# Performance work log

Hardware: AMD Instinct MI355X
Metric: run time of the kernel (lower is better)

Reference implementation:

```python
import jax, jax.numpy as jnp
import numpy as np

B, L, HID = 4, 2048, 2048
H, D = 16, 128
BASE = 10000.0
NEG = -1e30


def _rope_tables(seq_len, dim, dtype):
    # inv_freq: (dim/2,), emb = concat(freqs, freqs): (L, dim)
    inv_freq = 1.0 / (BASE ** (jnp.arange(0, dim, 2, dtype=jnp.float32) / dim))
    t = jnp.arange(seq_len, dtype=jnp.float32)
    freqs = t[:, None] * inv_freq[None, :]          # (L, dim/2)
    emb = jnp.concatenate([freqs, freqs], axis=-1)  # (L, dim)
    return jnp.cos(emb).astype(dtype), jnp.sin(emb).astype(dtype)


def _rotate_half(x):
    x1, x2 = x[..., : x.shape[-1] // 2], x[..., x.shape[-1] // 2 :]
    return jnp.concatenate([-x2, x1], axis=-1)


def setup_inputs() -> dict:
    key = jax.random.key(0)
    k1, k2, k3 = jax.random.split(key, 3)
    x = jax.random.normal(k1, (B, L, HID), dtype=jnp.float32)
    # qkv init std = sqrt(2/(5*hidden)); fc xavier std ~ sqrt(2/(in+out))
    Wqkv = jax.random.normal(k2, (HID, 3 * H * D), dtype=jnp.float32) * np.sqrt(2.0 / (5.0 * HID))
    Wo = jax.random.normal(k3, (H * D, HID), dtype=jnp.float32) * np.sqrt(2.0 / (H * D + HID))
    return {"x": x, "Wqkv": Wqkv, "Wo": Wo}


def reference(x, Wqkv, Wo):
    b, l, _ = x.shape
    qkv = (x @ Wqkv).reshape(b, l, 3, H, D).transpose(2, 0, 3, 1, 4)  # (3,b,h,l,d)
    q, k, v = qkv[0], qkv[1], qkv[2]
    cos, sin = _rope_tables(l, D, x.dtype)  # (l, D) each, broadcasts over (b,h,l,d)
    q = q * cos + _rotate_half(q) * sin
    k = k * cos + _rotate_half(k) * sin
    scale = 1.0 / np.sqrt(D)
    scores = jnp.einsum("bhqd,bhkd->bhqk", q, k) * scale  # (b,h,l,l)
    causal = jnp.tril(jnp.ones((l, l), dtype=bool))
    scores = jnp.where(causal, scores, NEG)
    att = jax.nn.softmax(scores, axis=-1)
    out = jnp.einsum("bhqk,bhkd->bhqd", att, v)  # (b,h,l,d)
    out = out.transpose(0, 2, 1, 3).reshape(b, l, H * D)
    return out @ Wo
```

## Files before the change

kernel.cpp:

```cpp
#include <hip/hip_runtime.h>
#include <hip/hip_bf16.h>
#include <stdint.h>

typedef unsigned short ushort_t;
typedef __bf16 bf16x8 __attribute__((ext_vector_type(8)));
typedef float    f32x4 __attribute__((ext_vector_type(4)));
typedef float   f32x16 __attribute__((ext_vector_type(16)));
typedef unsigned short us4 __attribute__((ext_vector_type(4)));
typedef unsigned int ui4 __attribute__((ext_vector_type(4)));

#define QK_SCALE 0.12751744f
#define NEG_BIG  -1e30f

#define BARRIER() do { asm volatile("" ::: "memory"); __builtin_amdgcn_s_barrier(); asm volatile("" ::: "memory"); } while (0)
#define VMCNT(N)  asm volatile("s_waitcnt vmcnt(" #N ")" ::: "memory")
#define MFMA16(d, a, b) d = __builtin_amdgcn_mfma_f32_16x16x32_bf16(a, b, d, 0, 0, 0)

__device__ __forceinline__ unsigned short f2bf(float f) {
    union { float f; unsigned int u; } v; v.f = f;
    unsigned int u = v.u;
    return (unsigned short)((u + 0x7FFFu + ((u >> 16) & 1u)) >> 16);
}

__device__ __forceinline__ unsigned int pk2bf(float a, float b) {
    unsigned int r;
    asm("v_cvt_pk_bf16_f32 %0, %1, %2" : "=v"(r) : "v"(a), "v"(b));
    return r;
}

__device__ __forceinline__ void gload16(const void* g, void* l) {
    __builtin_amdgcn_global_load_lds(
        (__attribute__((address_space(1))) void*)(uintptr_t)g,
        (__attribute__((address_space(3))) void*)(uint32_t)(uintptr_t)l,
        16, 0, 0);
}


__global__ __launch_bounds__(256) void cvt_bf16_kernel(
    const float4* __restrict__ in, us4* __restrict__ out, int n4) {
    int i = blockIdx.x * 256 + threadIdx.x;
    if (i >= n4) return;
    float4 v = in[i];
    us4 o; o[0] = f2bf(v.x); o[1] = f2bf(v.y); o[2] = f2bf(v.z); o[3] = f2bf(v.w);
    out[i] = o;
}

__global__ __launch_bounds__(256) void transpose_bf16(
    const float* __restrict__ in, ushort_t* __restrict__ out, int R, int C) {
    __shared__ float t[64][65];
    int c0 = blockIdx.x * 64, r0 = blockIdx.y * 64;
    int cc = threadIdx.x & 63, rr = threadIdx.x >> 6;
#pragma unroll
    for (int i = 0; i < 16; ++i) {
        int r = i * 4 + rr;
        t[r][cc] = in[(size_t)(r0 + r) * C + c0 + cc];
    }
    __syncthreads();
#pragma unroll
    for (int i = 0; i < 16; ++i) {
        int r = i * 4 + rr;
        out[(size_t)(c0 + r) * R + r0 + cc] = f2bf(t[cc][r]);
    }
}

__global__ __launch_bounds__(256) void transpose_wqkv(
    const float* __restrict__ in , ushort_t* __restrict__ out ) {
    __shared__ float t[64][65];
    int c0 = blockIdx.x * 64, r0 = blockIdx.y * 64;
    int cc = threadIdx.x & 63, rr = threadIdx.x >> 6;
    int n = c0 + cc;
    int which = n >> 11;
    int src = n;
    if (which < 2) {
        int h = (n >> 7) & 15, p = n & 127;
        int po = (p & 15) | (((p >> 5) & 3) << 4) | (((p >> 4) & 1) << 6);
        src = (which << 11) + (h << 7) + po;
    }
#pragma unroll
    for (int i = 0; i < 16; ++i) {
        int r = i * 4 + rr;
        t[r][cc] = in[(size_t)(r0 + r) * 6144 + src];
    }
    __syncthreads();
#pragma unroll
    for (int i = 0; i < 16; ++i) {
        int r = i * 4 + rr;
        out[(size_t)(c0 + r) * 2048 + r0 + cc] = f2bf(t[cc][r]);
    }
}

__global__ __launch_bounds__(256) void rope_table_kernel(float2* __restrict__ rope) {
    int i = blockIdx.x * 256 + threadIdx.x;
    int l = i >> 6, j = i & 63;
    float inv = exp2f((float)j * -0.20762050593046f);
    float f = (float)l * inv;
    rope[i] = make_float2(cosf(f), sinf(f));
}


template <int EPI>
__global__ __launch_bounds__(512, 2)
void gemm256(const ushort_t* __restrict__ A, const ushort_t* __restrict__ Bt,
             int M, int N, int K,
             float* __restrict__ C,
             ushort_t* __restrict__ Qb, ushort_t* __restrict__ Kb,
             ushort_t* __restrict__ Vt, const float2* __restrict__ rope) {
    __shared__ __attribute__((aligned(16))) char lds[131072];

    const int tid  = threadIdx.x;
    const int lane = tid & 63, wid = tid >> 6;
    const int lr = lane & 15, lg = lane >> 4;
    const int wr = wid >> 2, wc = wid & 3;

    const int nbn = N >> 8;
    const int nwg = gridDim.x;
    const int bid = blockIdx.x;
    const int wg  = (bid & 7) * (nwg >> 3) + (bid >> 3);
    const int bm  = wg / nbn, bn = wg % nbn;

    const int srow = tid >> 3;
    const int scol = ((tid & 7) << 4) ^ ((srow & 7) << 4);
    const size_t rowK2 = (size_t)K * 2;
    const char* sA0 = (const char*)A + ((size_t)(bm * 256 + srow)) * rowK2 + scol;
    const char* sA1 = sA0 + 128 * rowK2;
    const char* sB0 = (const char*)Bt + ((size_t)(bn * 256 + srow)) * rowK2 + scol;
    const char* sB1 = sB0 + 128 * rowK2;

    auto stg = [&](const char* s, int ch, int kt, int dst) {
        gload16(s + (size_t)(ch * 64) * rowK2 + (size_t)kt * 128, lds + dst + wid * 1024);
    };

    const int xk0 = (lg * 16) ^ ((lr & 7) << 4);
    const int xk1 = (64 + lg * 16) ^ ((lr & 7) << 4);
    const int rowA = wr * 16384 + lr * 128;
    const int rowB = 32768 + (wc >> 1) * 16384 + ((wc & 1) * 64 + lr) * 128;

    auto rdA = [&](int bu, int mi, int kk) -> bf16x8 {
        return *(const bf16x8*)(lds + bu * 65536 + rowA + mi * 2048 + (kk ? xk1 : xk0));
    };
    auto rdB = [&](int bu, int ni, int kk) -> bf16x8 {
        return *(const bf16x8*)(lds + bu * 65536 + rowB + ni * 2048 + (kk ? xk1 : xk0));
    };

    f32x4 acc[8][4];
#pragma unroll
    for (int m = 0; m < 8; ++m)
#pragma unroll
        for (int n = 0; n < 4; ++n) acc[m][n] = (f32x4){0.f, 0.f, 0.f, 0.f};

    bf16x8 aF[4][2], bF[2][2];

#define RD_A(BU, MH) do { _Pragma("unroll") for (int mi = 0; mi < 4; ++mi) { \
        aF[mi][0] = rdA(BU, (MH)*4 + mi, 0); aF[mi][1] = rdA(BU, (MH)*4 + mi, 1); } } while (0)
#define RD_B(BU, NH) do { _Pragma("unroll") for (int ni = 0; ni < 2; ++ni) { \
        bF[ni][0] = rdB(BU, (NH)*2 + ni, 0); bF[ni][1] = rdB(BU, (NH)*2 + ni, 1); } } while (0)
#define QUAD(MH, NH) do { __builtin_amdgcn_s_setprio(1); \
        _Pragma("unroll") for (int kk = 0; kk < 2; ++kk) \
        _Pragma("unroll") for (int mi = 0; mi < 4; ++mi) \
        _Pragma("unroll") for (int ni = 0; ni < 2; ++ni) \
            MFMA16(acc[(MH)*4 + mi][(NH)*2 + ni], aF[mi][kk], bF[ni][kk]); \
        __builtin_amdgcn_s_setprio(0); } while (0)

    stg(sA0, 0, 0, 0);     stg(sA0, 1, 0, 8192);
    stg(sA1, 0, 0, 16384); stg(sA1, 1, 0, 24576);
    stg(sB0, 0, 0, 32768); stg(sB0, 1, 0, 40960);
    stg(sB1, 0, 0, 49152); stg(sB1, 1, 0, 57344);
    stg(sA0, 1, 1, 73728); stg(sA1, 1, 1, 90112);
    stg(sB0, 0, 1, 98304); stg(sB0, 1, 1, 106496);
    VMCNT(4);
    BARRIER();

    const int NIT = K / 128;
    for (int i = 0; i < NIT; ++i) {
        const int to = 2 * i + 1, te2 = 2 * i + 2, to2 = 2 * i + 3;
        const bool g = (i + 1 < NIT);

        RD_A(0, 0); RD_B(0, 0);
        stg(sB1, 0, to, 114688); stg(sB1, 1, to, 122880);
        QUAD(0, 0); BARRIER();

        RD_A(0, 1);
        stg(sA0, 0, to, 65536); stg(sA1, 0, to, 81920);
        QUAD(1, 0); BARRIER();

        RD_B(0, 1);
        if (g) { stg(sA0, 1, te2, 8192); stg(sA1, 1, te2, 24576); }
        QUAD(1, 1); BARRIER();

        RD_A(0, 0);
        if (g) { stg(sB0, 0, te2, 32768); stg(sB0, 1, te2, 40960); VMCNT(4); }
        else   { VMCNT(0); }
        QUAD(0, 1); BARRIER();

        RD_A(1, 0); RD_B(1, 0);
        if (g) { stg(sB1, 0, te2, 49152); stg(sB1, 1, te2, 57344); }
        QUAD(0, 0); BARRIER();

        RD_A(1, 1);
        if (g) { stg(sA0, 0, te2, 0); stg(sA1, 0, te2, 16384); }
        QUAD(1, 0); BARRIER();

        RD_B(1, 1);
        if (g) { stg(sA0, 1, to2, 73728); stg(sA1, 1, to2, 90112); }
        QUAD(1, 1); BARRIER();

        RD_A(1, 0);
        if (g) { stg(sB0, 0, to2, 98304); stg(sB0, 1, to2, 106496); VMCNT(4); }
        QUAD(0, 1); BARRIER();
    }

#undef RD_A
#undef RD_B
#undef QUAD

    if constexpr (EPI == 0) {
#pragma unroll
        for (int m = 0; m < 8; ++m) {
            int gr0 = bm * 256 + wr * 128 + m * 16 + lg * 4;
#pragma unroll
            for (int n = 0; n < 4; ++n) {
                int gc = bn * 256 + wc * 64 + n * 16 + lr;
#pragma unroll
                for (int r = 0; r < 4; ++r)
                    C[(size_t)(gr0 + r) * N + gc] = acc[m][n][r];
            }
        }
    } else {
        const int hc = bn * 2 + (wc >> 1);
        const int which = hc >> 4, h = hc & 15;
#pragma unroll
        for (int m = 0; m < 8; ++m) {
            int gr0 = bm * 256 + wr * 128 + m * 16 + lg * 4;
            int b = gr0 >> 11, l0 = gr0 & 2047;
            if (which == 2) {
#pragma unroll
                for (int n = 0; n < 4; ++n) {
                    int d = (wc & 1) * 64 + n * 16 + lr;
                    us4 pk;
#pragma unroll
                    for (int r = 0; r < 4; ++r) pk[r] = f2bf(acc[m][n][r]);
                    *(us4*)(Vt + ((size_t)(b * 16 + h) * 128 + d) * 2048 + l0) = pk;
                }
            } else {
                ushort_t* dst = (which == 0) ? Qb : Kb;
                const float sc = (which == 0) ? QK_SCALE : 1.0f;
#pragma unroll
                for (int np = 0; np < 4; np += 2) {
                    int tbl = ((wc & 1) * 2 + (np >> 1)) * 16 + lr;
                    int p1 = (wc & 1) * 64 + np * 16 + lr;
#pragma unroll
                    for (int r = 0; r < 4; ++r) {
                        float2 cs = rope[(size_t)(l0 + r) * 64 + tbl];
                        float x1 = acc[m][np][r], x2 = acc[m][np + 1][r];
                        size_t base = ((size_t)(b * 16 + h) * 2048 + (l0 + r)) * 128;
                        dst[base + p1]      = f2bf((x1 * cs.x - x2 * cs.y) * sc);
                        dst[base + p1 + 16] = f2bf((x2 * cs.x + x1 * cs.y) * sc);
                    }
                }
            }
        }
    }
}


__global__ __attribute__((amdgpu_flat_work_group_size(512, 512), amdgpu_waves_per_eu(2, 2)))
void attn_fwd(const ushort_t* __restrict__ Qb, const ushort_t* __restrict__ Kb,
              const ushort_t* __restrict__ Vt, ushort_t* __restrict__ AO) {
    constexpr int L = 2048;
    __shared__ __attribute__((aligned(16))) char smem[131072];

    const int tid  = threadIdx.x;
    const int lane = tid & 63, wid = tid >> 6;
    const int q_l  = lane & 31;
    const int hi   = lane >> 5;

    const int bid  = blockIdx.x;
    const int hl   = (bid >> 3) & 7;
    const int pr   = bid >> 6;
    const int head = (bid & 7) * 8 + hl;

    const ushort_t* Qh = Qb + (size_t)head * L * 128;
    const char*     KhB = (const char*)(Kb + (size_t)head * L * 128);
    const char*     VhB = (const char*)(Vt + (size_t)head * 128 * L);
    const int b = head >> 4, h = head & 15;

    int rKV[4], cK[4], cV[4];
#pragma unroll
    for (int i = 0; i < 4; ++i) {
        rKV[i] = wid * 16 + i * 4 + (lane >> 4);
        cK[i]  = ((lane & 15) << 4) ^ ((rKV[i] & 7) << 4);
        cV[i]  = cK[i];
    }
    const int kdst = wid * 4096;
    const int vdst = 32768 + wid * 4096;

    for (int ph = 0; ph < 2; ++ph) {
        const int s    = ph ? (7 - pr) : pr;
        const int q0w  = s * 256 + wid * 32;
        const int nch  = 2 * s + 2;

        bf16x8 qf[8];
#pragma unroll
        for (int sb = 0; sb < 8; ++sb)
            qf[sb] = *(const bf16x8*)(Qh + (size_t)(q0w + q_l) * 128 + sb * 16 + hi * 8);

        f32x16 o[4];
#pragma unroll
        for (int d0 = 0; d0 < 4; ++d0) o[d0] = (f32x16)(0.f);
        float m_ = -__builtin_inff(), l_ = 0.f;

        __syncthreads();
#pragma unroll
        for (int i = 0; i < 4; ++i) {
            gload16(KhB + (size_t)rKV[i] * 256 + cK[i], smem + kdst + i * 1024);
            gload16(VhB + (size_t)rKV[i] * 4096 + cV[i], smem + vdst + i * 1024);
        }

        for (int c = 0; c < nch; ++c) {
            __syncthreads();
            const int kb = (c & 1) * 65536;
            const int nb = ((c + 1) & 1) * 65536;
            if (c + 1 < nch) {
                const int kn = 128 * (c + 1);
#pragma unroll
                for (int i = 0; i < 4; ++i) {
                    gload16(KhB + (size_t)(kn + rKV[i]) * 256 + cK[i], smem + nb + kdst + i * 1024);
                    gload16(VhB + (size_t)rKV[i] * 4096 + (size_t)kn * 2 + cV[i], smem + nb + vdst + i * 1024);
                }
            }

#pragma unroll
            for (int sub = 0; sub < 2; ++sub) {
                const int k0 = 128 * c + 64 * sub;
                if (k0 > q0w + 31) continue;
                const bool do1 = (k0 + 32 <= q0w + 31);
                const int kloc = sub * 64;

                f32x16 s0, s1;
                {
                    bf16x8 kf[8];
#pragma unroll
                    for (int sb = 0; sb < 8; ++sb) {
                        int off = kb + (kloc + q_l) * 256 + ((sb * 32 + hi * 16) ^ ((q_l & 7) << 4));
                        kf[sb] = *(const bf16x8*)(smem + off);
                    }
                    f32x16 sA = (f32x16)(0.f), sB = (f32x16)(0.f);
#pragma unroll
                    for (int sb = 0; sb < 8; sb += 2) {
                        sA = __builtin_amdgcn_mfma_f32_32x32x16_bf16(kf[sb],     qf[sb],     sA, 0, 0, 0);
                        sB = __builtin_amdgcn_mfma_f32_32x32x16_bf16(kf[sb + 1], qf[sb + 1], sB, 0, 0, 0);
                    }
                    s0 = sA + sB;
                }
                if (do1) {
                    bf16x8 kf[8];
#pragma unroll
                    for (int sb = 0; sb < 8; ++sb) {
                        int off = kb + (kloc + 32 + q_l) * 256 + ((sb * 32 + hi * 16) ^ ((q_l & 7) << 4));
                        kf[sb] = *(const bf16x8*)(smem + off);
                    }
                    f32x16 sA = (f32x16)(0.f), sB = (f32x16)(0.f);
#pragma unroll
                    for (int sb = 0; sb < 8; sb += 2) {
                        sA = __builtin_amdgcn_mfma_f32_32x32x16_bf16(kf[sb],     qf[sb],     sA, 0, 0, 0);
                        sB = __builtin_amdgcn_mfma_f32_32x32x16_bf16(kf[sb + 1], qf[sb + 1], sB, 0, 0, 0);
                    }
                    s1 = sA + sB;
                }

                if (k0 + 31 > q0w) {
#pragma unroll
                    for (int r = 0; r < 16; ++r) {
                        int crow = (r & 3) + 8 * (r >> 2) + 4 * hi;
                        if (k0 + crow > q0w + q_l) s0[r] = NEG_BIG;
                    }
                }
                if (do1 && (k0 + 63 > q0w)) {
#pragma unroll
                    for (int r = 0; r < 16; ++r) {
                        int crow = (r & 3) + 8 * (r >> 2) + 4 * hi;
                        if (k0 + 32 + crow > q0w + q_l) s1[r] = NEG_BIG;
                    }
                }

                float t8[8];
#pragma unroll
                for (int r = 0; r < 8; ++r) t8[r] = fmaxf(s0[r], s0[r + 8]);
                if (do1)
#pragma unroll
                    for (int r = 0; r < 8; ++r) t8[r] = fmaxf(t8[r], fmaxf(s1[r], s1[r + 8]));
#pragma unroll
                for (int r = 0; r < 4; ++r) t8[r] = fmaxf(t8[r], t8[r + 4]);
                float tmax = fmaxf(fmaxf(t8[0], t8[1]), fmaxf(t8[2], t8[3]));
                tmax = fmaxf(tmax, __shfl_xor(tmax, 32, 64));

                if (!__all(tmax <= m_ + 8.f)) {
                    float mn = fmaxf(m_, tmax);
                    float alpha = exp2f(m_ - mn);
                    m_ = mn;
                    l_ *= alpha;
#pragma unroll
                    for (int d0 = 0; d0 < 4; ++d0)
#pragma unroll
                        for (int r = 0; r < 16; ++r) o[d0][r] *= alpha;
                }

                float rs = 0.f;
#pragma unroll
                for (int r = 0; r < 16; ++r) { s0[r] = exp2f(s0[r] - m_); rs += s0[r]; }
                if (do1)
#pragma unroll
                    for (int r = 0; r < 16; ++r) { s1[r] = exp2f(s1[r] - m_); rs += s1[r]; }
                rs += __shfl_xor(rs, 32, 64);
                l_ += rs;

                bf16x8 pfA[2], pfB[2];
                {
                    unsigned int pk[8];
#pragma unroll
                    for (int i = 0; i < 8; ++i) pk[i] = pk2bf(s0[2 * i], s0[2 * i + 1]);
#pragma unroll
                    for (int ks = 0; ks < 2; ++ks) {
                        unsigned int a0 = pk[ks * 4 + 0], b0 = pk[ks * 4 + 2];
                        unsigned int a1 = pk[ks * 4 + 1], b1 = pk[ks * 4 + 3];
                        asm("v_permlane32_swap_b32 %0, %1" : "+v"(a0), "+v"(b0));
                        asm("v_permlane32_swap_b32 %0, %1" : "+v"(a1), "+v"(b1));
                        ui4 dw; dw[0] = a0; dw[1] = a1; dw[2] = b0; dw[3] = b1;
                        pfA[ks] = __builtin_bit_cast(bf16x8, dw);
                    }
                }
                if (do1) {
                    unsigned int pk[8];
#pragma unroll
                    for (int i = 0; i < 8; ++i) pk[i] = pk2bf(s1[2 * i], s1[2 * i + 1]);
#pragma unroll
                    for (int ks = 0; ks < 2; ++ks) {
                        unsigned int a0 = pk[ks * 4 + 0], b0 = pk[ks * 4 + 2];
                        unsigned int a1 = pk[ks * 4 + 1], b1 = pk[ks * 4 + 3];
                        asm("v_permlane32_swap_b32 %0, %1" : "+v"(a0), "+v"(b0));
                        asm("v_permlane32_swap_b32 %0, %1" : "+v"(a1), "+v"(b1));
                        ui4 dw; dw[0] = a0; dw[1] = a1; dw[2] = b0; dw[3] = b1;
                        pfB[ks] = __builtin_bit_cast(bf16x8, dw);
                    }
                }

                const int vb = kb + 32768;
#pragma unroll
                for (int d0 = 0; d0 < 4; ++d0) {
                    int d = d0 * 32 + q_l;
#pragma unroll
                    for (int ks = 0; ks < 2; ++ks) {
                        int off = vb + d * 256 + ((sub * 128 + ks * 32 + hi * 16) ^ ((d & 7) << 4));
                        bf16x8 vf = *(const bf16x8*)(smem + off);
                        o[d0] = __builtin_amdgcn_mfma_f32_32x32x16_bf16(vf, pfA[ks], o[d0], 0, 0, 0);
                    }
                    if (do1) {
#pragma unroll
                        for (int ks = 0; ks < 2; ++ks) {
                            int off = vb + d * 256 + ((sub * 128 + (2 + ks) * 32 + hi * 16) ^ ((d & 7) << 4));
                            bf16x8 vf = *(const bf16x8*)(smem + off);
                            o[d0] = __builtin_amdgcn_mfma_f32_32x32x16_bf16(vf, pfB[ks], o[d0], 0, 0, 0);
                        }
                    }
                }
            }
        }

        const float inv = 1.f / l_;
        const size_t rowbase = ((size_t)(b * 2048 + q0w + q_l)) * 2048 + h * 128;
#pragma unroll
        for (int d0 = 0; d0 < 4; ++d0)
#pragma unroll
            for (int g = 0; g < 4; ++g) {
                us4 v;
#pragma unroll
                for (int r = 0; r < 4; ++r) v[r] = f2bf(o[d0][g * 4 + r] * inv);
                *(us4*)(AO + rowbase + d0 * 32 + g * 8 + hi * 4) = v;
            }
    }
}


extern "C" void kernel_launch(void* const* d_in, const int* in_sizes, int n_in,
                              void* d_out, int out_size, void* d_ws, size_t ws_size,
                              hipStream_t stream) {
    const float* x    = (const float*)d_in[0];
    const float* Wqkv = (const float*)d_in[1];
    const float* Wo   = (const float*)d_in[2];
    float* out = (float*)d_out;

    char* w = (char*)d_ws;
    ushort_t* xb   = (ushort_t*)(w);
    ushort_t* W1t  = (ushort_t*)(w + 33554432);
    ushort_t* Wot  = (ushort_t*)(w + 58720256);
    ushort_t* Qb   = (ushort_t*)(w + 67108864);
    ushort_t* Kbf  = (ushort_t*)(w + 100663296);
    ushort_t* Vt   = (ushort_t*)(w + 134217728);
    ushort_t* AO   = (ushort_t*)(w + 167772160);
    float2*   rope = (float2*)(w + 201326592);

    cvt_bf16_kernel<<<16384, 256, 0, stream>>>((const float4*)x, (us4*)xb, 4194304);
    transpose_wqkv<<<dim3(96, 32), 256, 0, stream>>>(Wqkv, W1t);
    transpose_bf16<<<dim3(32, 32), 256, 0, stream>>>(Wo, Wot, 2048, 2048);
    rope_table_kernel<<<512, 256, 0, stream>>>(rope);

    gemm256<1><<<768, 512, 0, stream>>>(xb, W1t, 8192, 6144, 2048,
                                        nullptr, Qb, Kbf, Vt, rope);
    attn_fwd<<<256, 512, 0, stream>>>(Qb, Kbf, Vt, AO);
    gemm256<0><<<256, 512, 0, stream>>>(AO, Wot, 8192, 2048, 2048,
                                        out, nullptr, nullptr, nullptr, nullptr);
}
```

Baseline: 409.5 us.

## Merge prep kernels into one launch, prefetch V fragments, reorder GEMM LDS reads

The four preprocessing kernels (x conversion, Wqkv and Wo transposes, rope table) become a single launch that dispatches on block index, removing three kernel launches and the gaps between them. In attention, V fragments are read from LDS before the masking and softmax work, so LDS latency overlaps that math instead of sitting directly in front of the PV MFMAs. This raises register pressure (16 extra bf16x8 values) and could cut occupancy. The GEMM main loop also swaps the order of the A and B fragment reads.

```diff
diff --git a/kernel.cpp b/kernel.cpp
--- a/kernel.cpp
+++ b/kernel.cpp
@@ -35,66 +35,65 @@
         16, 0, 0);
 }
 
-
-__global__ __launch_bounds__(256) void cvt_bf16_kernel(
-    const float4* __restrict__ in, us4* __restrict__ out, int n4) {
-    int i = blockIdx.x * 256 + threadIdx.x;
-    if (i >= n4) return;
-    float4 v = in[i];
-    us4 o; o[0] = f2bf(v.x); o[1] = f2bf(v.y); o[2] = f2bf(v.z); o[3] = f2bf(v.w);
-    out[i] = o;
-}
-
-__global__ __launch_bounds__(256) void transpose_bf16(
-    const float* __restrict__ in, ushort_t* __restrict__ out, int R, int C) {
+__global__ __launch_bounds__(256) void prep_all(
+    const float* __restrict__ x, us4* __restrict__ xb4,
+    const float* __restrict__ Wqkv, ushort_t* __restrict__ W1t,
+    const float* __restrict__ Wo, ushort_t* __restrict__ Wot,
+    float2* __restrict__ rope) {
     __shared__ float t[64][65];
-    int c0 = blockIdx.x * 64, r0 = blockIdx.y * 64;
-    int cc = threadIdx.x & 63, rr = threadIdx.x >> 6;
-#pragma unroll
-    for (int i = 0; i < 16; ++i) {
-        int r = i * 4 + rr;
-        t[r][cc] = in[(size_t)(r0 + r) * C + c0 + cc];
+    const int blk = blockIdx.x;
+    const int tid = threadIdx.x;
+
+    if (blk < 16384) {
+        int i = blk * 256 + tid;
+        float4 v = ((const float4*)x)[i];
+        us4 o; o[0] = f2bf(v.x); o[1] = f2bf(v.y); o[2] = f2bf(v.z); o[3] = f2bf(v.w);
+        xb4[i] = o;
+    } else if (blk < 19456) {
+        int b2 = blk - 16384;
+        int c0 = (b2 % 96) * 64, r0 = (b2 / 96) * 64;
+        int cc = tid & 63, rr = tid >> 6;
+        int n = c0 + cc;
+        int which = n >> 11;
+        int src = n;
+        if (which < 2) {
+            int h = (n >> 7) & 15, p = n & 127;
+            int po = (p & 15) | (((p >> 5) & 3) << 4) | (((p >> 4) & 1) << 6);
+            src = (which << 11) + (h << 7) + po;
+        }
+#pragma unroll
+        for (int i = 0; i < 16; ++i) {
+            int r = i * 4 + rr;
+            t[r][cc] = Wqkv[(size_t)(r0 + r) * 6144 + src];
+        }
+        __syncthreads();
+#pragma unroll
+        for (int i = 0; i < 16; ++i) {
+            int r = i * 4 + rr;
+            W1t[(size_t)(c0 + r) * 2048 + r0 + cc] = f2bf(t[cc][r]);
+        }
+    } else if (blk < 20480) {
+        int b3 = blk - 19456;
+        int c0 = (b3 % 32) * 64, r0 = (b3 / 32) * 64;
+        int cc = tid & 63, rr = tid >> 6;
+#pragma unroll
+        for (int i = 0; i < 16; ++i) {
+            int r = i * 4 + rr;
+            t[r][cc] = Wo[(size_t)(r0 + r) * 2048 + c0 + cc];
+        }
+        __syncthreads();
+#pragma unroll
+        for (int i = 0; i < 16; ++i) {
+            int r = i * 4 + rr;
+            Wot[(size_t)(c0 + r) * 2048 + r0 + cc] = f2bf(t[cc][r]);
+        }
+    } else {
+        int i = (blk - 20480) * 256 + tid;
+        int l = i >> 6, j = i & 63;
+        float inv = exp2f((float)j * -0.20762050593046f);
+        float f = (float)l * inv;
+        rope[i] = make_float2(cosf(f), sinf(f));
     }
-    __syncthreads();
-#pragma unroll
-    for (int i = 0; i < 16; ++i) {
-        int r = i * 4 + rr;
-        out[(size_t)(c0 + r) * R + r0 + cc] = f2bf(t[cc][r]);
-    }
-}
-
-__global__ __launch_bounds__(256) void transpose_wqkv(
-    const float* __restrict__ in , ushort_t* __restrict__ out ) {
-    __shared__ float t[64][65];
-    int c0 = blockIdx.x * 64, r0 = blockIdx.y * 64;
-    int cc = threadIdx.x & 63, rr = threadIdx.x >> 6;
-    int n = c0 + cc;
-    int which = n >> 11;
-    int src = n;
-    if (which < 2) {
-        int h = (n >> 7) & 15, p = n & 127;
-        int po = (p & 15) | (((p >> 5) & 3) << 4) | (((p >> 4) & 1) << 6);
-        src = (which << 11) + (h << 7) + po;
-    }
-#pragma unroll
-    for (int i = 0; i < 16; ++i) {
-        int r = i * 4 + rr;
-        t[r][cc] = in[(size_t)(r0 + r) * 6144 + src];
-    }
-    __syncthreads();
-#pragma unroll
-    for (int i = 0; i < 16; ++i) {
-        int r = i * 4 + rr;
-        out[(size_t)(c0 + r) * 2048 + r0 + cc] = f2bf(t[cc][r]);
-    }
-}
-
-__global__ __launch_bounds__(256) void rope_table_kernel(float2* __restrict__ rope) {
-    int i = blockIdx.x * 256 + threadIdx.x;
-    int l = i >> 6, j = i & 63;
-    float inv = exp2f((float)j * -0.20762050593046f);
-    float f = (float)l * inv;
-    rope[i] = make_float2(cosf(f), sinf(f));
 }
 
 
@@ -175,7 +174,7 @@
         const int to = 2 * i + 1, te2 = 2 * i + 2, to2 = 2 * i + 3;
         const bool g = (i + 1 < NIT);
 
-        RD_A(0, 0); RD_B(0, 0);
+        RD_B(0, 0); RD_A(0, 0);
         stg(sB1, 0, to, 114688); stg(sB1, 1, to, 122880);
         QUAD(0, 0); BARRIER();
 
@@ -192,7 +191,7 @@
         else   { VMCNT(0); }
         QUAD(0, 1); BARRIER();
 
-        RD_A(1, 0); RD_B(1, 0);
+        RD_B(1, 0); RD_A(1, 0);
         if (g) { stg(sB1, 0, te2, 49152); stg(sB1, 1, te2, 57344); }
         QUAD(0, 0); BARRIER();
 
@@ -368,6 +367,29 @@
                     s1 = sA + sB;
                 }
 
+                const int vb = kb + 32768;
+                bf16x8 vfA[8], vfB[8];
+#pragma unroll
+                for (int d0 = 0; d0 < 4; ++d0) {
+                    int d = d0 * 32 + q_l;
+#pragma unroll
+                    for (int ks = 0; ks < 2; ++ks) {
+                        int offA = vb + d * 256 + ((sub * 128 + ks * 32 + hi * 16) ^ ((d & 7) << 4));
+                        vfA[d0 * 2 + ks] = *(const bf16x8*)(smem + offA);
+                    }
+                }
+                if (do1) {
+#pragma unroll
+                    for (int d0 = 0; d0 < 4; ++d0) {
+                        int d = d0 * 32 + q_l;
+#pragma unroll
+                        for (int ks = 0; ks < 2; ++ks) {
+                            int offB = vb + d * 256 + ((sub * 128 + (2 + ks) * 32 + hi * 16) ^ ((d & 7) << 4));
+                            vfB[d0 * 2 + ks] = *(const bf16x8*)(smem + offB);
+                        }
+                    }
+                }
+
                 if (k0 + 31 > q0w) {
 #pragma unroll
                     for (int r = 0; r < 16; ++r) {
@@ -444,24 +466,17 @@
                     }
                 }
 
-                const int vb = kb + 32768;
-#pragma unroll
-                for (int d0 = 0; d0 < 4; ++d0) {
-                    int d = d0 * 32 + q_l;
-#pragma unroll
-                    for (int ks = 0; ks < 2; ++ks) {
-                        int off = vb + d * 256 + ((sub * 128 + ks * 32 + hi * 16) ^ ((d & 7) << 4));
-                        bf16x8 vf = *(const bf16x8*)(smem + off);
-                        o[d0] = __builtin_amdgcn_mfma_f32_32x32x16_bf16(vf, pfA[ks], o[d0], 0, 0, 0);
-                    }
-                    if (do1) {
-#pragma unroll
-                        for (int ks = 0; ks < 2; ++ks) {
-                            int off = vb + d * 256 + ((sub * 128 + (2 + ks) * 32 + hi * 16) ^ ((d & 7) << 4));
-                            bf16x8 vf = *(const bf16x8*)(smem + off);
-                            o[d0] = __builtin_amdgcn_mfma_f32_32x32x16_bf16(vf, pfB[ks], o[d0], 0, 0, 0);
-                        }
-                    }
+#pragma unroll
+                for (int d0 = 0; d0 < 4; ++d0)
+#pragma unroll
+                    for (int ks = 0; ks < 2; ++ks)
+                        o[d0] = __builtin_amdgcn_mfma_f32_32x32x16_bf16(vfA[d0 * 2 + ks], pfA[ks], o[d0], 0, 0, 0);
+                if (do1) {
+#pragma unroll
+                    for (int d0 = 0; d0 < 4; ++d0)
+#pragma unroll
+                        for (int ks = 0; ks < 2; ++ks)
+                            o[d0] = __builtin_amdgcn_mfma_f32_32x32x16_bf16(vfB[d0 * 2 + ks], pfB[ks], o[d0], 0, 0, 0);
                 }
             }
         }
@@ -499,10 +514,7 @@
     ushort_t* AO   = (ushort_t*)(w + 167772160);
     float2*   rope = (float2*)(w + 201326592);
 
-    cvt_bf16_kernel<<<16384, 256, 0, stream>>>((const float4*)x, (us4*)xb, 4194304);
-    transpose_wqkv<<<dim3(96, 32), 256, 0, stream>>>(Wqkv, W1t);
-    transpose_bf16<<<dim3(32, 32), 256, 0, stream>>>(Wo, Wot, 2048, 2048);
-    rope_table_kernel<<<512, 256, 0, stream>>>(rope);
+    prep_all<<<20992, 256, 0, stream>>>(x, (us4*)xb, Wqkv, W1t, Wo, Wot, rope);
 
     gemm256<1><<<768, 512, 0, stream>>>(xb, W1t, 8192, 6144, 2048,
                                         nullptr, Qb, Kbf, Vt, rope);
```

New measurement: 455.5 us. 1.11x slower.
